# Kernel optimization log

Hardware: AMD Instinct MI355X
Metric: run time of the kernel (lower is better)

The kernel has to match this reference:

```python
import jax, jax.numpy as jnp
import numpy as np

K = 16  # matches init kwarg k


def setup_inputs() -> dict:
    key = jax.random.key(0)
    point_cloud = jax.random.normal(key, (4, 64, 4096), dtype=jnp.float32)
    return {"point_cloud": point_cloud}


def reference(point_cloud):
    B, dims, N = point_cloud.shape
    xt = jnp.transpose(point_cloud, (0, 2, 1))  # (B, N, dims)
    # pairwise euclidean distances (cdist, p=2)
    sq = jnp.sum(xt * xt, axis=-1)  # (B, N)
    d2 = sq[:, :, None] + sq[:, None, :] - 2.0 * jnp.einsum('bnd,bmd->bnm', xt, xt)
    dist = jnp.sqrt(jnp.maximum(d2, 0.0))  # (B, N, N)
    # k+1 smallest distances; drop self (first) neighbor
    _, idx_o = jax.lax.top_k(-dist, K + 1)  # (B, N, K+1)
    idx = idx_o[:, :, 1:]  # (B, N, K)
    # gather neighbor features: neighbors[b,d,n,j] = point_cloud[b,d,idx[b,n,j]]
    neighbors = jax.vmap(lambda pc, i: pc[:, i])(point_cloud, idx)  # (B, dims, N, K)
    central = point_cloud[:, :, :, None]  # (B, dims, N, 1)
    edge_feature = jnp.concatenate(
        [jnp.broadcast_to(central, (B, dims, N, K)), neighbors - central], axis=1
    )  # (B, 2*dims, N, K)
    return edge_feature, idx.reshape(B, -1)
```

## Files before the change

kernel.cpp:

```cpp
#include <hip/hip_runtime.h>


#define BATCH 4
#define DIMS 64
#define NPTS 4096
#define KNN 16
#define NCHUNK 32
#define CHLEN 128
#define GSZ 8
#define RN (BATCH * NPTS)
#define MLANES 8
#define MCH (NCHUNK / MLANES)
#define PBLK 512

typedef unsigned long long u64;
typedef unsigned int u32;

__device__ __forceinline__ double sentinel() {
    return __longlong_as_double(0x7FEFFFFFFFFFFFFFLL);
}

__global__ __launch_bounds__(256) void ef_sq_kernel(const float* __restrict__ pc,
                                                    float* __restrict__ sq) {
    int gid = blockIdx.x * 256 + threadIdx.x;
    int b = gid >> 12;
    int n = gid & (NPTS - 1);
    const float* p = pc + (size_t)b * DIMS * NPTS + n;
    float r[8];
#pragma unroll
    for (int j = 0; j < 8; ++j) {
        float v = p[(size_t)j * NPTS];
        r[j] = __fmul_rn(v, v);
    }
#pragma unroll
    for (int i = 8; i < DIMS; i += 8) {
#pragma unroll
        for (int j = 0; j < 8; ++j) {
            float v = p[(size_t)(i + j) * NPTS];
            r[j] = __fadd_rn(r[j], __fmul_rn(v, v));
        }
    }
    float t01 = __fadd_rn(r[0], r[1]);
    float t23 = __fadd_rn(r[2], r[3]);
    float t45 = __fadd_rn(r[4], r[5]);
    float t67 = __fadd_rn(r[6], r[7]);
    sq[gid] = __fadd_rn(__fadd_rn(t01, t23), __fadd_rn(t45, t67));
}

__global__ __launch_bounds__(256) void ef_transpose(const float* __restrict__ pc,
                                                    float* __restrict__ pcT) {
    __shared__ float smT[DIMS][65];
    int tid = threadIdx.x;
    int m0 = blockIdx.x * 64;
    int b = blockIdx.y;
    const float* pcb = pc + (size_t)b * DIMS * NPTS;
#pragma unroll
    for (int i = 0; i < 16; ++i) {
        int idx = i * 256 + tid;
        int d = idx >> 6;
        int m = idx & 63;
        smT[d][m] = pcb[(size_t)d * NPTS + m0 + m];
    }
    __syncthreads();
#pragma unroll
    for (int i = 0; i < 16; ++i) {
        int idx = i * 256 + tid;
        int m = idx >> 6;
        int d = idx & 63;
        pcT[((size_t)b * NPTS + m0 + m) * DIMS + d] = smT[d][m];
    }
}

__global__ __launch_bounds__(PBLK) void ef_knn_partial(const float* __restrict__ pc,
                                                       const float* __restrict__ sq,
                                                       u64* __restrict__ pKey) {
    __shared__ float tile[DIMS][CHLEN];
    __shared__ float tileSq[CHLEN];
    int tid = threadIdx.x;
    int r = blockIdx.x * PBLK + tid;
    int c = blockIdx.y;
    int b = (blockIdx.x * PBLK) >> 12;
    int n = r & (NPTS - 1);
    int m0 = c * CHLEN;
    const float* pcb = pc + (size_t)b * DIMS * NPTS;

    float xr[DIMS];
#pragma unroll
    for (int d = 0; d < DIMS; ++d) xr[d] = pcb[(size_t)d * NPTS + n];
#pragma unroll
    for (int d = 0; d < DIMS; ++d) asm volatile("" : "+v"(xr[d]));
    float sqn = sq[r];

#pragma unroll
    for (int i = 0; i < 4; ++i) {
        int idx = tid + i * PBLK;
        int d = idx >> 5;
        int mq = idx & 31;
        float4 v = *(const float4*)(pcb + (size_t)d * NPTS + m0 + mq * 4);
        *(float4*)&tile[d][mq * 4] = v;
    }
    if (tid < CHLEN / 4)
        *(float4*)&tileSq[tid * 4] =
            *(const float4*)(sq + (size_t)b * NPTS + m0 + tid * 4);
    __syncthreads();

    double key[KNN];
#pragma unroll
    for (int j = 0; j < KNN; ++j) key[j] = sentinel();

#define CE(arr, i, jj) { double lo_ = fmin(arr[i], arr[jj]); double hi_ = fmax(arr[i], arr[jj]); arr[i] = lo_; arr[jj] = hi_; }

    for (int g = 0; g < CHLEN; g += GSZ) {
        float acc[GSZ];
#pragma unroll
        for (int j = 0; j < GSZ; ++j) acc[j] = 0.f;
#pragma unroll
        for (int d = 0; d < DIMS; ++d) {
            float xv = xr[d];
            float4 lo = *(const float4*)&tile[d][g];
            float4 hi = *(const float4*)&tile[d][g + 4];
            acc[0] = fmaf(xv, lo.x, acc[0]);
            acc[1] = fmaf(xv, lo.y, acc[1]);
            acc[2] = fmaf(xv, lo.z, acc[2]);
            acc[3] = fmaf(xv, lo.w, acc[3]);
            acc[4] = fmaf(xv, hi.x, acc[4]);
            acc[5] = fmaf(xv, hi.y, acc[5]);
            acc[6] = fmaf(xv, hi.z, acc[6]);
            acc[7] = fmaf(xv, hi.w, acc[7]);
        }
        float4 sq_lo = *(const float4*)&tileSq[g];
        float4 sq_hi = *(const float4*)&tileSq[g + 4];
        float sqv[GSZ] = {sq_lo.x, sq_lo.y, sq_lo.z, sq_lo.w,
                          sq_hi.x, sq_hi.y, sq_hi.z, sq_hi.w};
        double s[GSZ];
#pragma unroll
        for (int j = 0; j < GSZ; ++j) {
            int m = m0 + g + j;
            float t1 = __fadd_rn(sqn, sqv[j]);
            float d2 = __fsub_rn(t1, __fmul_rn(2.0f, acc[j]));
            float dist = __fsqrt_rn(fmaxf(d2, 0.f));
            u64 cu = ((u64)__float_as_uint(dist) << 32) | (u64)(u32)m;
            double cand = __longlong_as_double((long long)cu);
            s[j] = (m == n) ? sentinel() : cand;
        }
        CE(s, 0, 1) CE(s, 2, 3) CE(s, 4, 5) CE(s, 6, 7)
        CE(s, 0, 2) CE(s, 1, 3) CE(s, 4, 6) CE(s, 5, 7)
        CE(s, 1, 2) CE(s, 5, 6)
        CE(s, 0, 4) CE(s, 1, 5) CE(s, 2, 6) CE(s, 3, 7)
        CE(s, 2, 4) CE(s, 3, 5)
        CE(s, 1, 2) CE(s, 3, 4) CE(s, 5, 6)
#pragma unroll
        for (int j = 8; j < 16; ++j) key[j] = fmin(key[j], s[15 - j]);
#pragma unroll
        for (int st = 8; st >= 1; st >>= 1) {
#pragma unroll
            for (int j = 0; j < KNN; ++j) {
                if ((j & st) == 0) {
                    double a = key[j], d = key[j | st];
                    key[j] = fmin(a, d);
                    key[j | st] = fmax(a, d);
                }
            }
        }
    }
#undef CE

    u64* dst = pKey + ((size_t)c * RN + r) * KNN;
#pragma unroll
    for (int j = 0; j < KNN; ++j) dst[j] = (u64)__double_as_longlong(key[j]);
}

__global__ __launch_bounds__(256) void ef_knn_merge(const u64* __restrict__ pKey,
                                                    float* __restrict__ outIdxF) {
    int t = blockIdx.x * 256 + threadIdx.x;
    int r = t >> 3;
    int s = t & 7;
    double key[KNN];
    {
        const u64* src = pKey + ((size_t)(s * MCH) * RN + r) * KNN;
#pragma unroll
        for (int j = 0; j < KNN; ++j)
            key[j] = __longlong_as_double((long long)src[j]);
    }
    for (int ci = 1; ci < MCH; ++ci) {
        const u64* src = pKey + ((size_t)(s * MCH + ci) * RN + r) * KNN;
        double v[KNN];
#pragma unroll
        for (int j = 0; j < KNN; ++j)
            v[j] = __longlong_as_double((long long)src[j]);
#pragma unroll
        for (int j = 0; j < KNN; ++j) key[j] = fmin(key[j], v[KNN - 1 - j]);
#pragma unroll
        for (int st = 8; st >= 1; st >>= 1) {
#pragma unroll
            for (int j = 0; j < KNN; ++j) {
                if ((j & st) == 0) {
                    double a = key[j], d = key[j | st];
                    key[j] = fmin(a, d);
                    key[j | st] = fmax(a, d);
                }
            }
        }
    }
#pragma unroll
    for (int mask = 1; mask <= 4; mask <<= 1) {
        double oth[KNN];
#pragma unroll
        for (int j = 0; j < KNN; ++j) oth[j] = __shfl_xor(key[j], mask, 64);
#pragma unroll
        for (int j = 0; j < KNN; ++j) key[j] = fmin(key[j], oth[KNN - 1 - j]);
#pragma unroll
        for (int st = 8; st >= 1; st >>= 1) {
#pragma unroll
            for (int j = 0; j < KNN; ++j) {
                if ((j & st) == 0) {
                    double a = key[j], d = key[j | st];
                    key[j] = fmin(a, d);
                    key[j | st] = fmax(a, d);
                }
            }
        }
    }
    if (s == 0) {
        float* dstf = outIdxF + (size_t)r * KNN;
#pragma unroll
        for (int j = 0; j < KNN; ++j)
            dstf[j] = (float)(u32)((u64)__double_as_longlong(key[j]) & 0xFFFFFFFFu);
    }
}

__global__ __launch_bounds__(256) void ef_edge_kernelT(const float* __restrict__ pcT,
                                                       const float* __restrict__ idxF,
                                                       float* __restrict__ out) {
    int t = blockIdx.x * 256 + threadIdx.x;
    int b = t >> 14;
    int rem = t & 16383;
    int n = rem >> 2;
    int k0 = (rem & 3) * 4;
    float4 i4 = *(const float4*)(idxF + (((size_t)(b << 12) + n) << 4) + k0);
    int m0 = (int)i4.x, m1 = (int)i4.y, m2 = (int)i4.z, m3 = (int)i4.w;
    const float4* cr  = (const float4*)(pcT + ((size_t)(b << 12) + n)  * DIMS);
    const float4* nr0 = (const float4*)(pcT + ((size_t)(b << 12) + m0) * DIMS);
    const float4* nr1 = (const float4*)(pcT + ((size_t)(b << 12) + m1) * DIMS);
    const float4* nr2 = (const float4*)(pcT + ((size_t)(b << 12) + m2) * DIMS);
    const float4* nr3 = (const float4*)(pcT + ((size_t)(b << 12) + m3) * DIMS);
    float* ob = out + (size_t)b * 2 * DIMS * NPTS * KNN + (size_t)n * KNN + k0;
#pragma unroll
    for (int q = 0; q < DIMS / 4; ++q) {
        float4 c4 = cr[q];
        float4 a0 = nr0[q], a1 = nr1[q], a2 = nr2[q], a3 = nr3[q];
        float cv, nv0, nv1, nv2, nv3;
        float4 st;
        cv = c4.x; nv0 = a0.x; nv1 = a1.x; nv2 = a2.x; nv3 = a3.x;
        st = make_float4(cv, cv, cv, cv);
        *(float4*)(ob + (size_t)(4 * q + 0) * (NPTS * KNN)) = st;
        st = make_float4(nv0 - cv, nv1 - cv, nv2 - cv, nv3 - cv);
        *(float4*)(ob + (size_t)(DIMS + 4 * q + 0) * (NPTS * KNN)) = st;
        cv = c4.y; nv0 = a0.y; nv1 = a1.y; nv2 = a2.y; nv3 = a3.y;
        st = make_float4(cv, cv, cv, cv);
        *(float4*)(ob + (size_t)(4 * q + 1) * (NPTS * KNN)) = st;
        st = make_float4(nv0 - cv, nv1 - cv, nv2 - cv, nv3 - cv);
        *(float4*)(ob + (size_t)(DIMS + 4 * q + 1) * (NPTS * KNN)) = st;
        cv = c4.z; nv0 = a0.z; nv1 = a1.z; nv2 = a2.z; nv3 = a3.z;
        st = make_float4(cv, cv, cv, cv);
        *(float4*)(ob + (size_t)(4 * q + 2) * (NPTS * KNN)) = st;
        st = make_float4(nv0 - cv, nv1 - cv, nv2 - cv, nv3 - cv);
        *(float4*)(ob + (size_t)(DIMS + 4 * q + 2) * (NPTS * KNN)) = st;
        cv = c4.w; nv0 = a0.w; nv1 = a1.w; nv2 = a2.w; nv3 = a3.w;
        st = make_float4(cv, cv, cv, cv);
        *(float4*)(ob + (size_t)(4 * q + 3) * (NPTS * KNN)) = st;
        st = make_float4(nv0 - cv, nv1 - cv, nv2 - cv, nv3 - cv);
        *(float4*)(ob + (size_t)(DIMS + 4 * q + 3) * (NPTS * KNN)) = st;
    }
}

__global__ __launch_bounds__(256) void ef_edge_kernel(const float* __restrict__ pc,
                                                      const float* __restrict__ idxF,
                                                      float* __restrict__ out) {
    int gid = blockIdx.x * 256 + threadIdx.x;
    int b = gid >> 16;
    int nk = gid & 65535;
    int n = nk >> 4;
    int m = (int)idxF[gid];
    const float* pcb = pc + (size_t)b * DIMS * NPTS;
    float* ob = out + (size_t)b * 2 * DIMS * NPTS * KNN;
#pragma unroll
    for (int d = 0; d < DIMS; ++d) {
        float cv = pcb[(size_t)d * NPTS + n];
        float nv = pcb[(size_t)d * NPTS + m];
        ob[(size_t)d * (NPTS * KNN) + nk] = cv;
        ob[(size_t)(DIMS + d) * (NPTS * KNN) + nk] = nv - cv;
    }
}

extern "C" void kernel_launch(void* const* d_in, const int* in_sizes, int n_in,
                              void* d_out, int out_size, void* d_ws, size_t ws_size,
                              hipStream_t stream) {
    const float* pc = (const float*)d_in[0];
    float* out = (float*)d_out;

    u64* pKey = (u64*)d_out;
    float* sq = out + 16777216;
    float* outIdxF = out + (size_t)BATCH * 2 * DIMS * NPTS * KNN;
    float* pcT = (float*)d_ws;
    bool useT = ws_size >= (size_t)BATCH * NPTS * DIMS * sizeof(float);

    ef_sq_kernel<<<(BATCH * NPTS) / 256, 256, 0, stream>>>(pc, sq);
    if (useT)
        ef_transpose<<<dim3(NPTS / 64, BATCH), 256, 0, stream>>>(pc, pcT);
    ef_knn_partial<<<dim3((BATCH * NPTS) / PBLK, NCHUNK), PBLK, 0, stream>>>(pc, sq, pKey);
    ef_knn_merge<<<(BATCH * NPTS * MLANES) / 256, 256, 0, stream>>>(pKey, outIdxF);
    if (useT)
        ef_edge_kernelT<<<(BATCH * NPTS * KNN / 4) / 256, 256, 0, stream>>>(pcT, outIdxF, out);
    else
        ef_edge_kernel<<<(BATCH * NPTS * KNN) / 256, 256, 0, stream>>>(pc, outIdxF, out);
}
```

Measured before the change: 323.0 us.

## Use packed FMA for distance dot products and split top-k sort between FP64 and integer compares

Rewrites the inner distance dot-product loop to use v_pk_fma_f32 on paired dimensions, which halves the FMA instruction count. The kNN partial kernel becomes templated so half the chunks sort their keys with FP64 min/max and the other half with 64-bit integer compares, launched as two grids. The intent is to spread compare-exchange work across the FP64 and integer ALU paths and to hint occupancy of 2 blocks per SM. Positive dist bit patterns order the same way as doubles or as u64, so the results match. The risks are extra launch overhead and register pressure from the launch bounds change.

```diff
diff --git a/kernel.cpp b/kernel.cpp
--- a/kernel.cpp
+++ b/kernel.cpp
@@ -15,9 +15,36 @@
 
 typedef unsigned long long u64;
 typedef unsigned int u32;
-
-__device__ __forceinline__ double sentinel() {
-    return __longlong_as_double(0x7FEFFFFFFFFFFFFFLL);
+typedef float f32x2 __attribute__((ext_vector_type(2)));
+typedef float f32x4 __attribute__((ext_vector_type(4)));
+
+#define SENT 0x7FEFFFFFFFFFFFFFULL
+
+template <bool F64>
+__device__ __forceinline__ void ce(u64& a, u64& b) {
+    if (F64) {
+        double da = __longlong_as_double((long long)a);
+        double db = __longlong_as_double((long long)b);
+        double lo = fmin(da, db), hi = fmax(da, db);
+        a = (u64)__double_as_longlong(lo);
+        b = (u64)__double_as_longlong(hi);
+    } else {
+        bool lt = a < b;
+        u64 lo = lt ? a : b;
+        u64 hi = lt ? b : a;
+        a = lo;
+        b = hi;
+    }
+}
+template <bool F64>
+__device__ __forceinline__ u64 keymin(u64 a, u64 b) {
+    if (F64) {
+        double m = fmin(__longlong_as_double((long long)a),
+                        __longlong_as_double((long long)b));
+        return (u64)__double_as_longlong(m);
+    } else {
+        return a < b ? a : b;
+    }
 }
 
 __global__ __launch_bounds__(256) void ef_sq_kernel(const float* __restrict__ pc,
@@ -71,24 +98,36 @@
     }
 }
 
-__global__ __launch_bounds__(PBLK) void ef_knn_partial(const float* __restrict__ pc,
-                                                       const float* __restrict__ sq,
-                                                       u64* __restrict__ pKey) {
+#define SHUF2(v, a, b) __builtin_shufflevector(v, v, a, b)
+#define PKFMA_LO(acc, xv, cv)                                                 \
+    asm("v_pk_fma_f32 %0, %1, %2, %0 op_sel:[0,0,0] op_sel_hi:[0,1,1]"        \
+        : "+v"(acc) : "v"(xv), "v"(cv))
+#define PKFMA_HI(acc, xv, cv)                                                 \
+    asm("v_pk_fma_f32 %0, %1, %2, %0 op_sel:[1,0,0] op_sel_hi:[1,1,1]"        \
+        : "+v"(acc) : "v"(xv), "v"(cv))
+
+template <bool F64>
+__global__ __launch_bounds__(PBLK, 2) void ef_knn_partial(const float* __restrict__ pc,
+                                                          const float* __restrict__ sq,
+                                                          u64* __restrict__ pKey,
+                                                          int c0) {
     __shared__ float tile[DIMS][CHLEN];
     __shared__ float tileSq[CHLEN];
     int tid = threadIdx.x;
     int r = blockIdx.x * PBLK + tid;
-    int c = blockIdx.y;
+    int c = c0 + blockIdx.y;
     int b = (blockIdx.x * PBLK) >> 12;
     int n = r & (NPTS - 1);
     int m0 = c * CHLEN;
     const float* pcb = pc + (size_t)b * DIMS * NPTS;
 
-    float xr[DIMS];
-#pragma unroll
-    for (int d = 0; d < DIMS; ++d) xr[d] = pcb[(size_t)d * NPTS + n];
-#pragma unroll
-    for (int d = 0; d < DIMS; ++d) asm volatile("" : "+v"(xr[d]));
+    f32x2 xp[DIMS / 2];
+#pragma unroll
+    for (int k = 0; k < DIMS / 2; ++k) {
+        float e = pcb[(size_t)(2 * k) * NPTS + n];
+        float o = pcb[(size_t)(2 * k + 1) * NPTS + n];
+        xp[k] = (f32x2){e, o};
+    }
     float sqn = sq[r];
 
 #pragma unroll
@@ -104,70 +143,65 @@
             *(const float4*)(sq + (size_t)b * NPTS + m0 + tid * 4);
     __syncthreads();
 
-    double key[KNN];
-#pragma unroll
-    for (int j = 0; j < KNN; ++j) key[j] = sentinel();
-
-#define CE(arr, i, jj) { double lo_ = fmin(arr[i], arr[jj]); double hi_ = fmax(arr[i], arr[jj]); arr[i] = lo_; arr[jj] = hi_; }
+    u64 key[KNN];
+#pragma unroll
+    for (int j = 0; j < KNN; ++j) key[j] = SENT;
 
     for (int g = 0; g < CHLEN; g += GSZ) {
-        float acc[GSZ];
-#pragma unroll
-        for (int j = 0; j < GSZ; ++j) acc[j] = 0.f;
-#pragma unroll
-        for (int d = 0; d < DIMS; ++d) {
-            float xv = xr[d];
-            float4 lo = *(const float4*)&tile[d][g];
-            float4 hi = *(const float4*)&tile[d][g + 4];
-            acc[0] = fmaf(xv, lo.x, acc[0]);
-            acc[1] = fmaf(xv, lo.y, acc[1]);
-            acc[2] = fmaf(xv, lo.z, acc[2]);
-            acc[3] = fmaf(xv, lo.w, acc[3]);
-            acc[4] = fmaf(xv, hi.x, acc[4]);
-            acc[5] = fmaf(xv, hi.y, acc[5]);
-            acc[6] = fmaf(xv, hi.z, acc[6]);
-            acc[7] = fmaf(xv, hi.w, acc[7]);
+        f32x2 accp[4];
+#pragma unroll
+        for (int j = 0; j < 4; ++j) accp[j] = (f32x2){0.f, 0.f};
+#pragma unroll
+        for (int k = 0; k < DIMS / 2; ++k) {
+            f32x4 qe0 = *(const f32x4*)&tile[2 * k][g];
+            f32x4 qe1 = *(const f32x4*)&tile[2 * k][g + 4];
+            f32x4 qo0 = *(const f32x4*)&tile[2 * k + 1][g];
+            f32x4 qo1 = *(const f32x4*)&tile[2 * k + 1][g + 4];
+            f32x2 xk = xp[k];
+            PKFMA_LO(accp[0], xk, SHUF2(qe0, 0, 1));
+            PKFMA_LO(accp[1], xk, SHUF2(qe0, 2, 3));
+            PKFMA_LO(accp[2], xk, SHUF2(qe1, 0, 1));
+            PKFMA_LO(accp[3], xk, SHUF2(qe1, 2, 3));
+            PKFMA_HI(accp[0], xk, SHUF2(qo0, 0, 1));
+            PKFMA_HI(accp[1], xk, SHUF2(qo0, 2, 3));
+            PKFMA_HI(accp[2], xk, SHUF2(qo1, 0, 1));
+            PKFMA_HI(accp[3], xk, SHUF2(qo1, 2, 3));
         }
         float4 sq_lo = *(const float4*)&tileSq[g];
         float4 sq_hi = *(const float4*)&tileSq[g + 4];
         float sqv[GSZ] = {sq_lo.x, sq_lo.y, sq_lo.z, sq_lo.w,
                           sq_hi.x, sq_hi.y, sq_hi.z, sq_hi.w};
-        double s[GSZ];
+        u64 s[GSZ];
 #pragma unroll
         for (int j = 0; j < GSZ; ++j) {
             int m = m0 + g + j;
+            float a = accp[j / 2][j % 2];
             float t1 = __fadd_rn(sqn, sqv[j]);
-            float d2 = __fsub_rn(t1, __fmul_rn(2.0f, acc[j]));
+            float d2 = __fsub_rn(t1, __fmul_rn(2.0f, a));
             float dist = __fsqrt_rn(fmaxf(d2, 0.f));
             u64 cu = ((u64)__float_as_uint(dist) << 32) | (u64)(u32)m;
-            double cand = __longlong_as_double((long long)cu);
-            s[j] = (m == n) ? sentinel() : cand;
-        }
-        CE(s, 0, 1) CE(s, 2, 3) CE(s, 4, 5) CE(s, 6, 7)
-        CE(s, 0, 2) CE(s, 1, 3) CE(s, 4, 6) CE(s, 5, 7)
-        CE(s, 1, 2) CE(s, 5, 6)
-        CE(s, 0, 4) CE(s, 1, 5) CE(s, 2, 6) CE(s, 3, 7)
-        CE(s, 2, 4) CE(s, 3, 5)
-        CE(s, 1, 2) CE(s, 3, 4) CE(s, 5, 6)
-#pragma unroll
-        for (int j = 8; j < 16; ++j) key[j] = fmin(key[j], s[15 - j]);
+            s[j] = (m == n) ? SENT : cu;
+        }
+        ce<F64>(s[0], s[1]); ce<F64>(s[2], s[3]); ce<F64>(s[4], s[5]); ce<F64>(s[6], s[7]);
+        ce<F64>(s[0], s[2]); ce<F64>(s[1], s[3]); ce<F64>(s[4], s[6]); ce<F64>(s[5], s[7]);
+        ce<F64>(s[1], s[2]); ce<F64>(s[5], s[6]);
+        ce<F64>(s[0], s[4]); ce<F64>(s[1], s[5]); ce<F64>(s[2], s[6]); ce<F64>(s[3], s[7]);
+        ce<F64>(s[2], s[4]); ce<F64>(s[3], s[5]);
+        ce<F64>(s[1], s[2]); ce<F64>(s[3], s[4]); ce<F64>(s[5], s[6]);
+#pragma unroll
+        for (int j = 8; j < 16; ++j) key[j] = keymin<F64>(key[j], s[15 - j]);
 #pragma unroll
         for (int st = 8; st >= 1; st >>= 1) {
 #pragma unroll
             for (int j = 0; j < KNN; ++j) {
-                if ((j & st) == 0) {
-                    double a = key[j], d = key[j | st];
-                    key[j] = fmin(a, d);
-                    key[j | st] = fmax(a, d);
-                }
+                if ((j & st) == 0) ce<F64>(key[j], key[j | st]);
             }
         }
     }
-#undef CE
 
     u64* dst = pKey + ((size_t)c * RN + r) * KNN;
 #pragma unroll
-    for (int j = 0; j < KNN; ++j) dst[j] = (u64)__double_as_longlong(key[j]);
+    for (int j = 0; j < KNN; ++j) dst[j] = key[j];
 }
 
 __global__ __launch_bounds__(256) void ef_knn_merge(const u64* __restrict__ pKey,
@@ -308,7 +342,8 @@
     ef_sq_kernel<<<(BATCH * NPTS) / 256, 256, 0, stream>>>(pc, sq);
     if (useT)
         ef_transpose<<<dim3(NPTS / 64, BATCH), 256, 0, stream>>>(pc, pcT);
-    ef_knn_partial<<<dim3((BATCH * NPTS) / PBLK, NCHUNK), PBLK, 0, stream>>>(pc, sq, pKey);
+    ef_knn_partial<true><<<dim3(RN / PBLK, NCHUNK / 2), PBLK, 0, stream>>>(pc, sq, pKey, 0);
+    ef_knn_partial<false><<<dim3(RN / PBLK, NCHUNK / 2), PBLK, 0, stream>>>(pc, sq, pKey, NCHUNK / 2);
     ef_knn_merge<<<(BATCH * NPTS * MLANES) / 256, 256, 0, stream>>>(pKey, outIdxF);
     if (useT)
         ef_edge_kernelT<<<(BATCH * NPTS * KNN / 4) / 256, 256, 0, stream>>>(pcT, outIdxF, out);
```

New measurement: 380.5 us. 17.8% more time.

## Process two chunks per KNN partial block, shuffle-only merge, split edge kernel by dims

Applied to the files above, without the earlier changes.

Each partial-KNN block now handles two 128-point chunks in sequence, which halves the number of partial top-k lists written to global memory (16 instead of 32). The merge kernel gives each of 16 lanes one list and combines them with shuffles only, removing the per-lane sequential loads and merges. The edge kernel is split across dimension groups, so each thread handles 4 dims instead of all 64, giving 16x more threads with less work each. In exchange the partial kernel launches half as many blocks, which lowers parallelism there, and the edge kernel reloads the neighbor indices once per dim group.

```diff
diff --git a/kernel.cpp b/kernel.cpp
--- a/kernel.cpp
+++ b/kernel.cpp
@@ -9,9 +9,10 @@
 #define CHLEN 128
 #define GSZ 8
 #define RN (BATCH * NPTS)
-#define MLANES 8
-#define MCH (NCHUNK / MLANES)
 #define PBLK 512
+#define CPB 2
+#define NLISTS (NCHUNK / CPB)
+#define MLANES 16
 
 typedef unsigned long long u64;
 typedef unsigned int u32;
@@ -78,10 +79,9 @@
     __shared__ float tileSq[CHLEN];
     int tid = threadIdx.x;
     int r = blockIdx.x * PBLK + tid;
-    int c = blockIdx.y;
+    int y = blockIdx.y;
     int b = (blockIdx.x * PBLK) >> 12;
     int n = r & (NPTS - 1);
-    int m0 = c * CHLEN;
     const float* pcb = pc + (size_t)b * DIMS * NPTS;
 
     float xr[DIMS];
@@ -91,66 +91,108 @@
     for (int d = 0; d < DIMS; ++d) asm volatile("" : "+v"(xr[d]));
     float sqn = sq[r];
 
-#pragma unroll
-    for (int i = 0; i < 4; ++i) {
-        int idx = tid + i * PBLK;
-        int d = idx >> 5;
-        int mq = idx & 31;
-        float4 v = *(const float4*)(pcb + (size_t)d * NPTS + m0 + mq * 4);
-        *(float4*)&tile[d][mq * 4] = v;
-    }
-    if (tid < CHLEN / 4)
-        *(float4*)&tileSq[tid * 4] =
-            *(const float4*)(sq + (size_t)b * NPTS + m0 + tid * 4);
-    __syncthreads();
-
     double key[KNN];
 #pragma unroll
     for (int j = 0; j < KNN; ++j) key[j] = sentinel();
 
 #define CE(arr, i, jj) { double lo_ = fmin(arr[i], arr[jj]); double hi_ = fmax(arr[i], arr[jj]); arr[i] = lo_; arr[jj] = hi_; }
 
-    for (int g = 0; g < CHLEN; g += GSZ) {
-        float acc[GSZ];
-#pragma unroll
-        for (int j = 0; j < GSZ; ++j) acc[j] = 0.f;
-#pragma unroll
-        for (int d = 0; d < DIMS; ++d) {
-            float xv = xr[d];
-            float4 lo = *(const float4*)&tile[d][g];
-            float4 hi = *(const float4*)&tile[d][g + 4];
-            acc[0] = fmaf(xv, lo.x, acc[0]);
-            acc[1] = fmaf(xv, lo.y, acc[1]);
-            acc[2] = fmaf(xv, lo.z, acc[2]);
-            acc[3] = fmaf(xv, lo.w, acc[3]);
-            acc[4] = fmaf(xv, hi.x, acc[4]);
-            acc[5] = fmaf(xv, hi.y, acc[5]);
-            acc[6] = fmaf(xv, hi.z, acc[6]);
-            acc[7] = fmaf(xv, hi.w, acc[7]);
-        }
-        float4 sq_lo = *(const float4*)&tileSq[g];
-        float4 sq_hi = *(const float4*)&tileSq[g + 4];
-        float sqv[GSZ] = {sq_lo.x, sq_lo.y, sq_lo.z, sq_lo.w,
-                          sq_hi.x, sq_hi.y, sq_hi.z, sq_hi.w};
-        double s[GSZ];
-#pragma unroll
-        for (int j = 0; j < GSZ; ++j) {
-            int m = m0 + g + j;
-            float t1 = __fadd_rn(sqn, sqv[j]);
-            float d2 = __fsub_rn(t1, __fmul_rn(2.0f, acc[j]));
-            float dist = __fsqrt_rn(fmaxf(d2, 0.f));
-            u64 cu = ((u64)__float_as_uint(dist) << 32) | (u64)(u32)m;
-            double cand = __longlong_as_double((long long)cu);
-            s[j] = (m == n) ? sentinel() : cand;
-        }
-        CE(s, 0, 1) CE(s, 2, 3) CE(s, 4, 5) CE(s, 6, 7)
-        CE(s, 0, 2) CE(s, 1, 3) CE(s, 4, 6) CE(s, 5, 7)
-        CE(s, 1, 2) CE(s, 5, 6)
-        CE(s, 0, 4) CE(s, 1, 5) CE(s, 2, 6) CE(s, 3, 7)
-        CE(s, 2, 4) CE(s, 3, 5)
-        CE(s, 1, 2) CE(s, 3, 4) CE(s, 5, 6)
-#pragma unroll
-        for (int j = 8; j < 16; ++j) key[j] = fmin(key[j], s[15 - j]);
+    for (int t = 0; t < CPB; ++t) {
+        int m0 = (y * CPB + t) * CHLEN;
+        if (t) __syncthreads();
+#pragma unroll
+        for (int i = 0; i < 4; ++i) {
+            int idx = tid + i * PBLK;
+            int d = idx >> 5;
+            int mq = idx & 31;
+            float4 v = *(const float4*)(pcb + (size_t)d * NPTS + m0 + mq * 4);
+            *(float4*)&tile[d][mq * 4] = v;
+        }
+        if (tid < CHLEN / 4)
+            *(float4*)&tileSq[tid * 4] =
+                *(const float4*)(sq + (size_t)b * NPTS + m0 + tid * 4);
+        __syncthreads();
+
+        for (int g = 0; g < CHLEN; g += GSZ) {
+            float acc[GSZ];
+#pragma unroll
+            for (int j = 0; j < GSZ; ++j) acc[j] = 0.f;
+#pragma unroll
+            for (int d = 0; d < DIMS; ++d) {
+                float xv = xr[d];
+                float4 lo = *(const float4*)&tile[d][g];
+                float4 hi = *(const float4*)&tile[d][g + 4];
+                acc[0] = fmaf(xv, lo.x, acc[0]);
+                acc[1] = fmaf(xv, lo.y, acc[1]);
+                acc[2] = fmaf(xv, lo.z, acc[2]);
+                acc[3] = fmaf(xv, lo.w, acc[3]);
+                acc[4] = fmaf(xv, hi.x, acc[4]);
+                acc[5] = fmaf(xv, hi.y, acc[5]);
+                acc[6] = fmaf(xv, hi.z, acc[6]);
+                acc[7] = fmaf(xv, hi.w, acc[7]);
+            }
+            float4 sq_lo = *(const float4*)&tileSq[g];
+            float4 sq_hi = *(const float4*)&tileSq[g + 4];
+            float sqv[GSZ] = {sq_lo.x, sq_lo.y, sq_lo.z, sq_lo.w,
+                              sq_hi.x, sq_hi.y, sq_hi.z, sq_hi.w};
+            double s[GSZ];
+#pragma unroll
+            for (int j = 0; j < GSZ; ++j) {
+                int m = m0 + g + j;
+                float t1 = __fadd_rn(sqn, sqv[j]);
+                float d2 = __fsub_rn(t1, __fmul_rn(2.0f, acc[j]));
+                float dist = __fsqrt_rn(fmaxf(d2, 0.f));
+                u64 cu = ((u64)__float_as_uint(dist) << 32) | (u64)(u32)m;
+                double cand = __longlong_as_double((long long)cu);
+                s[j] = (m == n) ? sentinel() : cand;
+            }
+            CE(s, 0, 1) CE(s, 2, 3) CE(s, 4, 5) CE(s, 6, 7)
+            CE(s, 0, 2) CE(s, 1, 3) CE(s, 4, 6) CE(s, 5, 7)
+            CE(s, 1, 2) CE(s, 5, 6)
+            CE(s, 0, 4) CE(s, 1, 5) CE(s, 2, 6) CE(s, 3, 7)
+            CE(s, 2, 4) CE(s, 3, 5)
+            CE(s, 1, 2) CE(s, 3, 4) CE(s, 5, 6)
+#pragma unroll
+            for (int j = 8; j < 16; ++j) key[j] = fmin(key[j], s[15 - j]);
+#pragma unroll
+            for (int st = 8; st >= 1; st >>= 1) {
+#pragma unroll
+                for (int j = 0; j < KNN; ++j) {
+                    if ((j & st) == 0) {
+                        double a = key[j], d = key[j | st];
+                        key[j] = fmin(a, d);
+                        key[j | st] = fmax(a, d);
+                    }
+                }
+            }
+        }
+    }
+#undef CE
+
+    u64* dst = pKey + ((size_t)y * RN + r) * KNN;
+#pragma unroll
+    for (int j = 0; j < KNN; ++j) dst[j] = (u64)__double_as_longlong(key[j]);
+}
+
+__global__ __launch_bounds__(256) void ef_knn_merge(const u64* __restrict__ pKey,
+                                                    float* __restrict__ outIdxF) {
+    int t = blockIdx.x * 256 + threadIdx.x;
+    int r = t >> 4;
+    int s = t & 15;
+    double key[KNN];
+    {
+        const u64* src = pKey + ((size_t)s * RN + r) * KNN;
+#pragma unroll
+        for (int j = 0; j < KNN; ++j)
+            key[j] = __longlong_as_double((long long)src[j]);
+    }
+#pragma unroll
+    for (int mask = 1; mask <= 8; mask <<= 1) {
+        double oth[KNN];
+#pragma unroll
+        for (int j = 0; j < KNN; ++j) oth[j] = __shfl_xor(key[j], mask, 64);
+#pragma unroll
+        for (int j = 0; j < KNN; ++j) key[j] = fmin(key[j], oth[KNN - 1 - j]);
 #pragma unroll
         for (int st = 8; st >= 1; st >>= 1) {
 #pragma unroll
@@ -163,64 +205,6 @@
             }
         }
     }
-#undef CE
-
-    u64* dst = pKey + ((size_t)c * RN + r) * KNN;
-#pragma unroll
-    for (int j = 0; j < KNN; ++j) dst[j] = (u64)__double_as_longlong(key[j]);
-}
-
-__global__ __launch_bounds__(256) void ef_knn_merge(const u64* __restrict__ pKey,
-                                                    float* __restrict__ outIdxF) {
-    int t = blockIdx.x * 256 + threadIdx.x;
-    int r = t >> 3;
-    int s = t & 7;
-    double key[KNN];
-    {
-        const u64* src = pKey + ((size_t)(s * MCH) * RN + r) * KNN;
-#pragma unroll
-        for (int j = 0; j < KNN; ++j)
-            key[j] = __longlong_as_double((long long)src[j]);
-    }
-    for (int ci = 1; ci < MCH; ++ci) {
-        const u64* src = pKey + ((size_t)(s * MCH + ci) * RN + r) * KNN;
-        double v[KNN];
-#pragma unroll
-        for (int j = 0; j < KNN; ++j)
-            v[j] = __longlong_as_double((long long)src[j]);
-#pragma unroll
-        for (int j = 0; j < KNN; ++j) key[j] = fmin(key[j], v[KNN - 1 - j]);
-#pragma unroll
-        for (int st = 8; st >= 1; st >>= 1) {
-#pragma unroll
-            for (int j = 0; j < KNN; ++j) {
-                if ((j & st) == 0) {
-                    double a = key[j], d = key[j | st];
-                    key[j] = fmin(a, d);
-                    key[j | st] = fmax(a, d);
-                }
-            }
-        }
-    }
-#pragma unroll
-    for (int mask = 1; mask <= 4; mask <<= 1) {
-        double oth[KNN];
-#pragma unroll
-        for (int j = 0; j < KNN; ++j) oth[j] = __shfl_xor(key[j], mask, 64);
-#pragma unroll
-        for (int j = 0; j < KNN; ++j) key[j] = fmin(key[j], oth[KNN - 1 - j]);
-#pragma unroll
-        for (int st = 8; st >= 1; st >>= 1) {
-#pragma unroll
-            for (int j = 0; j < KNN; ++j) {
-                if ((j & st) == 0) {
-                    double a = key[j], d = key[j | st];
-                    key[j] = fmin(a, d);
-                    key[j | st] = fmax(a, d);
-                }
-            }
-        }
-    }
     if (s == 0) {
         float* dstf = outIdxF + (size_t)r * KNN;
 #pragma unroll
@@ -232,46 +216,40 @@
 __global__ __launch_bounds__(256) void ef_edge_kernelT(const float* __restrict__ pcT,
                                                        const float* __restrict__ idxF,
                                                        float* __restrict__ out) {
-    int t = blockIdx.x * 256 + threadIdx.x;
-    int b = t >> 14;
-    int rem = t & 16383;
+    int gid = blockIdx.x * 256 + threadIdx.x;
+    int u = gid & 65535;
+    int q = gid >> 16;
+    int b = u >> 14;
+    int rem = u & 16383;
     int n = rem >> 2;
     int k0 = (rem & 3) * 4;
-    float4 i4 = *(const float4*)(idxF + (((size_t)(b << 12) + n) << 4) + k0);
+    float4 i4 = *(const float4*)(idxF + (((size_t)b << 12) + n) * KNN + k0);
     int m0 = (int)i4.x, m1 = (int)i4.y, m2 = (int)i4.z, m3 = (int)i4.w;
-    const float4* cr  = (const float4*)(pcT + ((size_t)(b << 12) + n)  * DIMS);
-    const float4* nr0 = (const float4*)(pcT + ((size_t)(b << 12) + m0) * DIMS);
-    const float4* nr1 = (const float4*)(pcT + ((size_t)(b << 12) + m1) * DIMS);
-    const float4* nr2 = (const float4*)(pcT + ((size_t)(b << 12) + m2) * DIMS);
-    const float4* nr3 = (const float4*)(pcT + ((size_t)(b << 12) + m3) * DIMS);
-    float* ob = out + (size_t)b * 2 * DIMS * NPTS * KNN + (size_t)n * KNN + k0;
-#pragma unroll
-    for (int q = 0; q < DIMS / 4; ++q) {
-        float4 c4 = cr[q];
-        float4 a0 = nr0[q], a1 = nr1[q], a2 = nr2[q], a3 = nr3[q];
-        float cv, nv0, nv1, nv2, nv3;
-        float4 st;
-        cv = c4.x; nv0 = a0.x; nv1 = a1.x; nv2 = a2.x; nv3 = a3.x;
-        st = make_float4(cv, cv, cv, cv);
-        *(float4*)(ob + (size_t)(4 * q + 0) * (NPTS * KNN)) = st;
-        st = make_float4(nv0 - cv, nv1 - cv, nv2 - cv, nv3 - cv);
-        *(float4*)(ob + (size_t)(DIMS + 4 * q + 0) * (NPTS * KNN)) = st;
-        cv = c4.y; nv0 = a0.y; nv1 = a1.y; nv2 = a2.y; nv3 = a3.y;
-        st = make_float4(cv, cv, cv, cv);
-        *(float4*)(ob + (size_t)(4 * q + 1) * (NPTS * KNN)) = st;
-        st = make_float4(nv0 - cv, nv1 - cv, nv2 - cv, nv3 - cv);
-        *(float4*)(ob + (size_t)(DIMS + 4 * q + 1) * (NPTS * KNN)) = st;
-        cv = c4.z; nv0 = a0.z; nv1 = a1.z; nv2 = a2.z; nv3 = a3.z;
-        st = make_float4(cv, cv, cv, cv);
-        *(float4*)(ob + (size_t)(4 * q + 2) * (NPTS * KNN)) = st;
-        st = make_float4(nv0 - cv, nv1 - cv, nv2 - cv, nv3 - cv);
-        *(float4*)(ob + (size_t)(DIMS + 4 * q + 2) * (NPTS * KNN)) = st;
-        cv = c4.w; nv0 = a0.w; nv1 = a1.w; nv2 = a2.w; nv3 = a3.w;
-        st = make_float4(cv, cv, cv, cv);
-        *(float4*)(ob + (size_t)(4 * q + 3) * (NPTS * KNN)) = st;
-        st = make_float4(nv0 - cv, nv1 - cv, nv2 - cv, nv3 - cv);
-        *(float4*)(ob + (size_t)(DIMS + 4 * q + 3) * (NPTS * KNN)) = st;
-    }
+    const float* base = pcT + (((size_t)b << 12)) * DIMS + q * 4;
+    float4 c4 = *(const float4*)(base + (size_t)n * DIMS);
+    float4 a0 = *(const float4*)(base + (size_t)m0 * DIMS);
+    float4 a1 = *(const float4*)(base + (size_t)m1 * DIMS);
+    float4 a2 = *(const float4*)(base + (size_t)m2 * DIMS);
+    float4 a3 = *(const float4*)(base + (size_t)m3 * DIMS);
+    float* ob = out + ((size_t)b * 2 * DIMS + 4 * q) * (NPTS * KNN)
+                    + (size_t)n * KNN + k0;
+    float cv;
+    cv = c4.x;
+    *(float4*)(ob + 0 * (size_t)(NPTS * KNN)) = make_float4(cv, cv, cv, cv);
+    *(float4*)(ob + (size_t)(DIMS + 0) * (NPTS * KNN)) =
+        make_float4(a0.x - cv, a1.x - cv, a2.x - cv, a3.x - cv);
+    cv = c4.y;
+    *(float4*)(ob + 1 * (size_t)(NPTS * KNN)) = make_float4(cv, cv, cv, cv);
+    *(float4*)(ob + (size_t)(DIMS + 1) * (NPTS * KNN)) =
+        make_float4(a0.y - cv, a1.y - cv, a2.y - cv, a3.y - cv);
+    cv = c4.z;
+    *(float4*)(ob + 2 * (size_t)(NPTS * KNN)) = make_float4(cv, cv, cv, cv);
+    *(float4*)(ob + (size_t)(DIMS + 2) * (NPTS * KNN)) =
+        make_float4(a0.z - cv, a1.z - cv, a2.z - cv, a3.z - cv);
+    cv = c4.w;
+    *(float4*)(ob + 3 * (size_t)(NPTS * KNN)) = make_float4(cv, cv, cv, cv);
+    *(float4*)(ob + (size_t)(DIMS + 3) * (NPTS * KNN)) =
+        make_float4(a0.w - cv, a1.w - cv, a2.w - cv, a3.w - cv);
 }
 
 __global__ __launch_bounds__(256) void ef_edge_kernel(const float* __restrict__ pc,
@@ -308,10 +286,10 @@
     ef_sq_kernel<<<(BATCH * NPTS) / 256, 256, 0, stream>>>(pc, sq);
     if (useT)
         ef_transpose<<<dim3(NPTS / 64, BATCH), 256, 0, stream>>>(pc, pcT);
-    ef_knn_partial<<<dim3((BATCH * NPTS) / PBLK, NCHUNK), PBLK, 0, stream>>>(pc, sq, pKey);
-    ef_knn_merge<<<(BATCH * NPTS * MLANES) / 256, 256, 0, stream>>>(pKey, outIdxF);
+    ef_knn_partial<<<dim3(RN / PBLK, NLISTS), PBLK, 0, stream>>>(pc, sq, pKey);
+    ef_knn_merge<<<(RN * MLANES) / 256, 256, 0, stream>>>(pKey, outIdxF);
     if (useT)
-        ef_edge_kernelT<<<(BATCH * NPTS * KNN / 4) / 256, 256, 0, stream>>>(pcT, outIdxF, out);
+        ef_edge_kernelT<<<(BATCH * NPTS * KNN * 16 / 4) / 256, 256, 0, stream>>>(pcT, outIdxF, out);
     else
         ef_edge_kernel<<<(BATCH * NPTS * KNN) / 256, 256, 0, stream>>>(pc, outIdxF, out);
 }
```

Result: slower. 363.2 us (+12.5%).
